# Performance work log

Measured on AMD Instinct MI355X. Metric: run time of the kernel, lower is better.

Reference implementation:

```python
import jax, jax.numpy as jnp
import numpy as np

IN_FEATURES = 8192
OUT_FEATURES = 512
N_BITS = 8
ABS_RANGE = 4.0
TOP_K = 32
SIZE = IN_FEATURES // N_BITS            # per-bit latent/weight slice size
QUANT_STEP = ABS_RANGE / 2 ** N_BITS
BATCH = 4096


def setup_inputs() -> dict:
    key = jax.random.key(0)
    k1, k2, k3 = jax.random.split(key, 3)
    lim = float(np.sqrt(6.0 / (IN_FEATURES + OUT_FEATURES)))  # xavier_uniform
    latent = jax.random.normal(k1, (BATCH, IN_FEATURES), jnp.float32)
    weight = jax.random.uniform(k2, (IN_FEATURES, OUT_FEATURES), jnp.float32, -lim, lim)
    weight_mirror = jax.random.uniform(k3, (IN_FEATURES, OUT_FEATURES), jnp.float32, -lim, lim)
    return {"latent": latent, "weight": weight, "weight_mirror": weight_mirror}


def _forward(latent, weight, weight_mirror):
    sg = jax.lax.stop_gradient
    B = latent.shape[0]
    # reshape into per-bit slices: latent [B, n_bits, size], weights [n_bits, size, out]
    L = latent.reshape(B, N_BITS, SIZE)
    Wn = weight.reshape(N_BITS, SIZE, OUT_FEATURES)
    Wm = weight_mirror.reshape(N_BITS, SIZE, OUT_FEATURES)
    # sign binarization with straight-through estimator (forward = sign, grad = identity)
    Bsign = sg(jnp.where(Wn >= 0, 1.0, -1.0).astype(Wn.dtype))
    Bsign_m = sg(jnp.where(Wm >= 0, 1.0, -1.0).astype(Wm.dtype))
    Wsum = sg(Bsign + Bsign_m - Wn - Wm) + Wn + Wm  # ste_weight + ste_weight_mirror
    # top-k sparsify each slice, then STE sign of surviving entries
    k = min(TOP_K, SIZE)
    if TOP_K is not None and TOP_K > 0 and k < SIZE:
        _, idx = jax.lax.top_k(L, k)                       # [B, n_bits, k]
        mask = jnp.zeros(L.shape, bool)
        b = jnp.arange(B)[:, None, None]
        n = jnp.arange(N_BITS)[None, :, None]
        mask = mask.at[b, n, idx].set(True)
        Lm = L * mask
        Ls = sg(jnp.sign(Lm) - Lm) + Lm                    # forward = sign(masked), grad = mask
    else:
        Ls = L
    # per-bit scale: 2**(n_bits-i-2) * quant_step
    scales = (2.0 ** (N_BITS - jnp.arange(N_BITS) - 2)).astype(latent.dtype) * jnp.asarray(QUANT_STEP, latent.dtype)
    contrib = jnp.einsum('bns,nso->bno', Ls, Wsum) * scales[None, :, None]  # [B, n_bits, out]
    # reconstruction_i = detach(reconstruction_{i-1}) + contrib_i  ->  detached prefix cumsum
    cum = jnp.cumsum(sg(contrib), axis=1) - sg(contrib) + contrib
    result = jnp.transpose(cum, (1, 0, 2))                 # [n_bits, B, out]
    latent_group = jnp.mean(jnp.sum(jnp.abs(Ls), axis=-1), axis=0)  # [n_bits]
    return latent_group, result


def reference(latent, weight, weight_mirror):
    return _forward(latent, weight, weight_mirror)
```

## Files before the change

### kernel.cpp

```cpp
#include <hip/hip_runtime.h>
#include <stdint.h>

#define NBITS  8
#define SLICE  1024
#define OUTF   512
#define INF    8192
#define TOPK   32
#define BATCHN 4096

#define ROWS    INF
#define DUMMY_B (ROWS * 64 * 4)
#define TBL2_B  ((ROWS + 1) * 64 * 4)

__device__ __forceinline__ uint32_t fkey_u(uint32_t u) {
  uint32_t m = ((uint32_t)((int32_t)u >> 31)) | 0x80000000u;
  return u ^ m;
}
__device__ __forceinline__ float kfloat(uint32_t k) {
  uint32_t u = (k & 0x80000000u) ? (k ^ 0x80000000u) : ~k;
  return __uint_as_float(u);
}

__global__ __launch_bounds__(256) void prep_kernel(
    const float* __restrict__ W, const float* __restrict__ Wm,
    uint32_t* __restrict__ tbl)
{
  int tid = blockIdx.x * blockDim.x + threadIdx.x;
  int r = tid >> 6;
  int w = tid & 63;
  const float* wr = W  + (size_t)r * OUTF;
  const float* mr = Wm + (size_t)r * OUTF;
  uint32_t word = 0;
#pragma unroll
  for (int i = 0; i < 8; ++i) {
    int col = w + 64 * i;
    uint32_t b = (wr[col] >= 0.0f ? 1u : 0u) + (mr[col] >= 0.0f ? 1u : 0u);
    word |= b << (4 * i);
  }
  tbl[tid] = word;
  tbl[(TBL2_B / 4) + tid] = 0x22222222u - word;
  if (tid < 64) tbl[(DUMMY_B / 4) + tid] = 0x11111111u;
}

__global__ __launch_bounds__(512, 4) void main_kernel(
    const float* __restrict__ latent,
    const uint32_t* __restrict__ tbl,
    float* __restrict__ out, int* __restrict__ partial)
{
  __shared__ __align__(16) uint32_t sel[NBITS][TOPK];
  __shared__ float sums[NBITS][OUTF];

  const int b    = blockIdx.x;
  const int wv   = threadIdx.x >> 6;
  const int lane = threadIdx.x & 63;

  const float4* src =
      (const float4*)(latent + (size_t)b * INF + (size_t)wv * SLICE + lane * 16);
  uint32_t key[16];
  uint32_t lmax = 0u;
#pragma unroll
  for (int q = 0; q < 4; ++q) {
    float4 f = src[q];
    float vv[4] = {f.x, f.y, f.z, f.w};
#pragma unroll
    for (int t = 0; t < 4; ++t) {
      uint32_t k = fkey_u(__float_as_uint(vv[t]));
      key[4*q+t] = k;
      lmax = lmax > k ? lmax : k;
    }
  }

  uint32_t bmin = lmax, bmax = lmax;
#pragma unroll
  for (int d = 1; d < 64; d <<= 1) {
    uint32_t tn = (uint32_t)__shfl_xor((int)bmin, d);
    uint32_t tx = (uint32_t)__shfl_xor((int)bmax, d);
    bmin = bmin < tn ? bmin : tn;
    bmax = bmax > tx ? bmax : tx;
  }

  uint32_t T = 0, midE = 0, cE = 0;
  bool fast = false;
  {
    uint32_t lo = bmin, hi = bmax;
    while (lo < hi) {
      uint32_t d   = hi - lo;
      uint32_t mid = lo + (d >> 1) + (d & 1u);
      float fm     = 0.5f * (kfloat(lo) + kfloat(hi));
      uint32_t km  = fkey_u(__float_as_uint(fm));
      if (km > lo && km <= hi) mid = km;
      uint32_t c = 0;
#pragma unroll
      for (int j = 0; j < 16; ++j) c += (key[j] >= mid) ? 1u : 0u;
      int cnt = 0;
#pragma unroll
      for (int bb = 0; bb < 5; ++bb)
        cnt += (int)__popcll(__ballot((c >> bb) & 1u)) << bb;
      if (cnt == TOPK) { fast = true; midE = mid; cE = c; break; }
      if (cnt > TOPK) lo = mid; else hi = mid - 1u;
    }
    if (!fast) T = lo;
  }

  const uint32_t pbase = ((uint32_t)(wv * SLICE + lane * 16)) << 8;
  int nzl = 0;

  if (fast) {
    int sc = (int)cE;
#pragma unroll
    for (int dd = 1; dd < 64; dd <<= 1) {
      int t = __shfl_up(sc, dd);
      if (lane >= dd) sc += t;
    }
    int slot = sc - (int)cE;
#pragma unroll
    for (int j = 0; j < 16; ++j) {
      uint32_t kk = key[j];
      if (kk >= midE) {
        bool ispos = kk > 0x80000000u;
        bool isneg = kk < 0x7FFFFFFFu;
        uint32_t off = ispos ? (pbase + (j << 8))
                     : (isneg ? (pbase + (j << 8) + TBL2_B) : (uint32_t)DUMMY_B);
        sel[wv][slot++] = off;
        nzl += (ispos || isneg) ? 1 : 0;
      }
    }
  } else {
    int cgt = 0, ceq = 0;
#pragma unroll
    for (int j = 0; j < 16; ++j) { cgt += (key[j] > T); ceq += (key[j] == T); }
    int packed = (cgt << 16) | ceq;
    int sc = packed;
#pragma unroll
    for (int dd = 1; dd < 64; dd <<= 1) {
      int t = __shfl_up(sc, dd);
      if (lane >= dd) sc += t;
    }
    int tot     = __shfl(sc, 63);
    int total_g = tot >> 16;
    int nties   = TOPK - total_g;
    int excl    = sc - packed;
    int posg    = excl >> 16;
    int pose    = excl & 0xFFFF;
#pragma unroll
    for (int j = 0; j < 16; ++j) {
      uint32_t kk  = key[j];
      bool isgt    = kk > T;
      bool iseq    = (kk == T);
      bool takeeq  = iseq && (pose < nties);
      bool take    = isgt || takeeq;
      bool ispos   = kk > 0x80000000u;
      bool isneg   = kk < 0x7FFFFFFFu;
      uint32_t off = ispos ? (pbase + (j << 8))
                   : (isneg ? (pbase + (j << 8) + TBL2_B) : (uint32_t)DUMMY_B);
      int slot = isgt ? posg : (total_g + pose);
      if (take) sel[wv][slot] = off;
      posg += isgt ? 1 : 0;
      pose += iseq ? 1 : 0;
      nzl  += (take && (ispos || isneg)) ? 1 : 0;
    }
  }

  {
    int cnz = 0;
#pragma unroll
    for (int bb = 0; bb < 5; ++bb)
      cnz += (int)__popcll(__ballot((nzl >> bb) & 1)) << bb;
    if (lane == 0) partial[wv * BATCHN + b] = cnz;
  }

  uint32_t offr[TOPK];
  {
    const uint4* sp = (const uint4*)sel[wv];
#pragma unroll
    for (int q = 0; q < TOPK / 4; ++q) {
      uint4 e4 = sp[q];
      offr[4*q+0] = e4.x; offr[4*q+1] = e4.y;
      offr[4*q+2] = e4.z; offr[4*q+3] = e4.w;
    }
  }
  const uint32_t lb = (uint32_t)lane << 2;
  const char* tbase = (const char*)tbl;
  uint32_t wrd[TOPK];
#pragma unroll
  for (int j = 0; j < TOPK; ++j)
    wrd[j] = *(const uint32_t*)(tbase + (offr[j] + lb));
  __builtin_amdgcn_sched_barrier(0);

  uint32_t acc0 = 0, acc1 = 0, tmp = 0;
  int inch = 0;
#pragma unroll
  for (int j = 0; j < TOPK; ++j) {
    tmp += wrd[j];
    if (++inch == 7 || j == TOPK - 1) {
      acc0 += tmp & 0x0F0F0F0Fu;
      acc1 += (tmp >> 4) & 0x0F0F0F0Fu;
      tmp = 0; inch = 0;
    }
  }

  const float scale_n = 1.0f / (float)(1 << wv);
#pragma unroll
  for (int i2 = 0; i2 < 4; ++i2) {
    int f0 = (int)((acc0 >> (8 * i2)) & 0xFFu);
    int f1 = (int)((acc1 >> (8 * i2)) & 0xFFu);
    sums[wv][lane + 128 * i2]      = scale_n * (float)(2 * f0 - 64);
    sums[wv][lane + 128 * i2 + 64] = scale_n * (float)(2 * f1 - 64);
  }

  __syncthreads();

  const int col = threadIdx.x;
  float racc = 0.0f;
  float* obase = out + 8 + (size_t)b * OUTF + col;
#pragma unroll
  for (int n2 = 0; n2 < NBITS; ++n2) {
    racc += sums[n2][col];
    obase[(size_t)n2 * BATCHN * OUTF] = racc;
  }
}

__global__ __launch_bounds__(512) void fin_kernel(
    const int* __restrict__ partial, float* __restrict__ out)
{
  const int wv   = threadIdx.x >> 6;
  const int lane = threadIdx.x & 63;
  const int* p = partial + wv * BATCHN;
  int s = 0;
#pragma unroll
  for (int k = 0; k < BATCHN / 64; ++k)
    s += p[lane + 64 * k];
#pragma unroll
  for (int d = 32; d >= 1; d >>= 1)
    s += __shfl_down(s, d);
  if (lane == 0) out[wv] = (float)s * (1.0f / (float)BATCHN);
}

extern "C" void kernel_launch(void* const* d_in, const int* in_sizes, int n_in,
                              void* d_out, int out_size, void* d_ws, size_t ws_size,
                              hipStream_t stream)
{
  const float* latent = (const float*)d_in[0];
  const float* W      = (const float*)d_in[1];
  const float* Wm     = (const float*)d_in[2];
  float* out = (float*)d_out;

  int*      partial = (int*)d_ws;
  uint32_t* tbl     = (uint32_t*)((char*)d_ws + 131072);

  prep_kernel<<<(INF * 64) / 256, 256, 0, stream>>>(W, Wm, tbl);
  main_kernel<<<BATCHN, 512, 0, stream>>>(latent, tbl, out, partial);
  fin_kernel<<<1, 512, 0, stream>>>(partial, out);
}
```

Baseline: 70.99 us.

## Use log-interpolated threshold search, fuse final reduction via ticket, adjust occupancy

Replaces the midpoint bisection for the top-k threshold with an interpolation step that uses the log of the previous counts (assuming roughly Gaussian tails), with a bisection fallback. The count loop is split into four independent accumulators. The separate final reduction kernel is removed: the last block to finish, detected with an atomic ticket, performs the latent_group reduction. Launch bounds drop from 4 to 3 waves per SIMD. These aim to cut search iterations and one kernel launch, at the cost of an extra atomic and block barrier in every block.

Result: slower. 202.4 us (+185.1%).

```diff
diff --git a/kernel.cpp b/kernel.cpp
--- a/kernel.cpp
+++ b/kernel.cpp
@@ -23,9 +23,10 @@
 
 __global__ __launch_bounds__(256) void prep_kernel(
     const float* __restrict__ W, const float* __restrict__ Wm,
-    uint32_t* __restrict__ tbl)
+    uint32_t* __restrict__ tbl, int* __restrict__ ticket)
 {
   int tid = blockIdx.x * blockDim.x + threadIdx.x;
+  if (tid == 0) *ticket = 0;
   int r = tid >> 6;
   int w = tid & 63;
   const float* wr = W  + (size_t)r * OUTF;
@@ -42,13 +43,15 @@
   if (tid < 64) tbl[(DUMMY_B / 4) + tid] = 0x11111111u;
 }
 
-__global__ __launch_bounds__(512, 4) void main_kernel(
+__global__ __launch_bounds__(512, 3) void main_kernel(
     const float* __restrict__ latent,
     const uint32_t* __restrict__ tbl,
-    float* __restrict__ out, int* __restrict__ partial)
+    float* __restrict__ out, int* __restrict__ partial,
+    int* __restrict__ ticket)
 {
   __shared__ __align__(16) uint32_t sel[NBITS][TOPK];
   __shared__ float sums[NBITS][OUTF];
+  __shared__ int   islast;
 
   const int b    = blockIdx.x;
   const int wv   = threadIdx.x >> 6;
@@ -83,21 +86,33 @@
   bool fast = false;
   {
     uint32_t lo = bmin, hi = bmax;
+    float flo = kfloat(lo), fhi = kfloat(hi);
+    float llo = 6.0f, lhi = 0.0f;
+    const float l32 = 3.4657359f;
     while (lo < hi) {
-      uint32_t d   = hi - lo;
-      uint32_t mid = lo + (d >> 1) + (d & 1u);
-      float fm     = 0.5f * (kfloat(lo) + kfloat(hi));
-      uint32_t km  = fkey_u(__float_as_uint(fm));
+      float fr = (l32 - lhi) / (llo - lhi);
+      fr = fminf(fmaxf(fr, 0.06f), 0.94f);
+      uint32_t km = fkey_u(__float_as_uint(fhi + fr * (flo - fhi)));
+      uint32_t mid;
       if (km > lo && km <= hi) mid = km;
-      uint32_t c = 0;
-#pragma unroll
-      for (int j = 0; j < 16; ++j) c += (key[j] >= mid) ? 1u : 0u;
+      else { uint32_t d = hi - lo; mid = lo + (d >> 1) + (d & 1u); }
+      uint32_t c0 = 0, c1 = 0, c2 = 0, c3 = 0;
+#pragma unroll
+      for (int j = 0; j < 4; ++j) {
+        c0 += (key[j]      >= mid) ? 1u : 0u;
+        c1 += (key[j + 4]  >= mid) ? 1u : 0u;
+        c2 += (key[j + 8]  >= mid) ? 1u : 0u;
+        c3 += (key[j + 12] >= mid) ? 1u : 0u;
+      }
+      uint32_t c = (c0 + c1) + (c2 + c3);
       int cnt = 0;
 #pragma unroll
       for (int bb = 0; bb < 5; ++bb)
         cnt += (int)__popcll(__ballot((c >> bb) & 1u)) << bb;
       if (cnt == TOPK) { fast = true; midE = mid; cE = c; break; }
-      if (cnt > TOPK) lo = mid; else hi = mid - 1u;
+      float lc = __logf((float)(cnt > 0 ? cnt : 1));
+      if (cnt > TOPK) { lo = mid;      flo = kfloat(lo); llo = lc; }
+      else            { hi = mid - 1u; fhi = kfloat(hi); lhi = lc; }
     }
     if (!fast) T = lo;
   }
@@ -184,7 +199,7 @@
   uint32_t wrd[TOPK];
 #pragma unroll
   for (int j = 0; j < TOPK; ++j)
-    wrd[j] = *(const uint32_t*)(tbase + (offr[j] + lb));
+    wrd[j] = *(const uint32_t*)(tbase + (size_t)(offr[j] + lb));
   __builtin_amdgcn_sched_barrier(0);
 
   uint32_t acc0 = 0, acc1 = 0, tmp = 0;
@@ -218,22 +233,26 @@
     racc += sums[n2][col];
     obase[(size_t)n2 * BATCHN * OUTF] = racc;
   }
-}
-
-__global__ __launch_bounds__(512) void fin_kernel(
-    const int* __restrict__ partial, float* __restrict__ out)
-{
-  const int wv   = threadIdx.x >> 6;
-  const int lane = threadIdx.x & 63;
-  const int* p = partial + wv * BATCHN;
-  int s = 0;
-#pragma unroll
-  for (int k = 0; k < BATCHN / 64; ++k)
-    s += p[lane + 64 * k];
-#pragma unroll
-  for (int d = 32; d >= 1; d >>= 1)
-    s += __shfl_down(s, d);
-  if (lane == 0) out[wv] = (float)s * (1.0f / (float)BATCHN);
+
+  __syncthreads();
+  if (threadIdx.x == 0) {
+    __threadfence();
+    int old = atomicAdd(ticket, 1);
+    islast = (old == (int)gridDim.x - 1) ? 1 : 0;
+  }
+  __syncthreads();
+  if (islast) {
+    __threadfence();
+    const int* p = partial + wv * BATCHN;
+    int s = 0;
+#pragma unroll
+    for (int k = 0; k < BATCHN / 64; ++k)
+      s += p[lane + 64 * k];
+#pragma unroll
+    for (int d = 32; d >= 1; d >>= 1)
+      s += __shfl_down(s, d);
+    if (lane == 0) out[wv] = (float)s * (1.0f / (float)BATCHN);
+  }
 }
 
 extern "C" void kernel_launch(void* const* d_in, const int* in_sizes, int n_in,
@@ -246,9 +265,9 @@
   float* out = (float*)d_out;
 
   int*      partial = (int*)d_ws;
-  uint32_t* tbl     = (uint32_t*)((char*)d_ws + 131072);
-
-  prep_kernel<<<(INF * 64) / 256, 256, 0, stream>>>(W, Wm, tbl);
-  main_kernel<<<BATCHN, 512, 0, stream>>>(latent, tbl, out, partial);
-  fin_kernel<<<1, 512, 0, stream>>>(partial, out);
-}
+  int*      ticket  = (int*)((char*)d_ws + 131072);
+  uint32_t* tbl     = (uint32_t*)((char*)d_ws + 131328);
+
+  prep_kernel<<<(INF * 64) / 256, 256, 0, stream>>>(W, Wm, tbl, ticket);
+  main_kernel<<<BATCHN, 512, 0, stream>>>(latent, tbl, out, partial, ticket);
+}
```
